# Kernel tuning notes

Measured on AMD Instinct MI355X. Metric: run time of the kernel, lower is better.

The kernel has to match this reference:

```python
import jax, jax.numpy as jnp
import numpy as np

D = 384      # d_model
H = 12       # num_heads
DK = 32      # head dim
L = 6        # num_layers
FF = 1536    # FFN intermediate (4*d_model)
EPS = 1e-12  # BERT LayerNorm eps


def layer_norm(x, w, b):
    m = jnp.mean(x, -1, keepdims=True)
    v = jnp.mean((x - m) ** 2, -1, keepdims=True)
    return (x - m) * jax.lax.rsqrt(v + EPS) * w + b


def deltanet(x, mask, Wq, bq, Wk, bk, Wv, bv, Wb, bb, Wg, bg, Wo, bo, fl, sl):
    # Hierarchical delta-rule linear attention with fast/slow decay states.
    B, S, _ = x.shape
    q = (x @ Wq + bq).reshape(B, S, H, DK)
    k = (x @ Wk + bk).reshape(B, S, H, DK)
    k = k / (jnp.linalg.norm(k, axis=-1, keepdims=True) + 1e-6)
    v = (x @ Wv + bv).reshape(B, S, H, DK)
    beta = jax.nn.sigmoid(x @ Wb + bb) * mask[:, :, None]   # [B,S,H] write gate
    g = jax.nn.sigmoid(x @ Wg + bg)                          # [B,S,H] flux mix gate
    af = jax.nn.sigmoid(fl)[None, :, None, None]             # fast decay, init 0.3
    as_ = jax.nn.sigmoid(sl)[None, :, None, None]            # slow decay, init 0.85

    def step(carry, inp):
        Sf, Ss = carry                      # [B,H,DK,DK] states
        qt, kt, vt, bt, gt = inp            # [B,H,DK],[B,H,DK],[B,H,DK],[B,H],[B,H]
        rf = jnp.einsum('bhkd,bhk->bhd', Sf, kt)
        Sf = af * Sf + bt[..., None, None] * kt[..., :, None] * (vt - rf)[:, :, None, :]
        of = jnp.einsum('bhkd,bhk->bhd', Sf, qt)
        rs = jnp.einsum('bhkd,bhk->bhd', Ss, kt)
        Ss = as_ * Ss + bt[..., None, None] * kt[..., :, None] * (vt - rs)[:, :, None, :]
        os_ = jnp.einsum('bhkd,bhk->bhd', Ss, qt)
        out = gt[..., None] * of + (1.0 - gt[..., None]) * os_
        return (Sf, Ss), out

    to_t = lambda a: jnp.moveaxis(a, 1, 0)  # [B,S,...] -> [S,B,...]
    S0 = jnp.zeros((B, H, DK, DK), x.dtype)
    _, out = jax.lax.scan(step, (S0, S0), (to_t(q), to_t(k), to_t(v), to_t(beta), to_t(g)))
    out = jnp.moveaxis(out, 0, 1).reshape(B, S, D)
    return out @ Wo + bo


def _forward(input_ids, attention_mask, word_emb, pos_emb, type_emb, emb_ln_w, emb_ln_b,
             Wq, bq, Wk, bk, Wv, bv, Wbeta, bbeta, Wg, bg, Wo, bo, fast_logit, slow_logit,
             attn_ln_w, attn_ln_b, ffn_w1, ffn_b1, ffn_w2, ffn_b2, ffn_ln_w, ffn_ln_b):
    B, S = input_ids.shape
    mask = attention_mask.astype(jnp.float32)
    x = word_emb[input_ids] + pos_emb[:S][None] + type_emb[0][None, None]
    x = layer_norm(x, emb_ln_w, emb_ln_b)
    for i in range(L):
        res = x
        a = deltanet(x, mask, Wq[i], bq[i], Wk[i], bk[i], Wv[i], bv[i],
                     Wbeta[i], bbeta[i], Wg[i], bg[i], Wo[i], bo[i],
                     fast_logit[i], slow_logit[i])
        x = layer_norm(res + a, attn_ln_w[i], attn_ln_b[i])
        res = x
        h = jax.nn.gelu(x @ ffn_w1[i] + ffn_b1[i], approximate=False)
        x = layer_norm(res + h @ ffn_w2[i] + ffn_b2[i], ffn_ln_w[i], ffn_ln_b[i])
    m = mask[:, :, None]
    emb = jnp.sum(x * m, 1) / jnp.clip(jnp.sum(m, 1), 1e-9)
    return emb / jnp.linalg.norm(emb, axis=1, keepdims=True)


def setup_inputs() -> dict:
    key = jax.random.key(0)
    ks = jax.random.split(key, 16)
    B, S, V, P = 64, 512, 30522, 512
    n = lambda k, shp, s=0.02: jax.random.normal(k, shp, jnp.float32) * s
    return {
        'input_ids': jax.random.randint(ks[0], (B, S), 0, V),
        'attention_mask': jnp.ones((B, S), jnp.int32),
        'word_emb': n(ks[1], (V, D)),
        'pos_emb': n(ks[2], (P, D)),
        'type_emb': n(ks[3], (2, D)),
        'emb_ln_w': jnp.ones((D,)), 'emb_ln_b': jnp.zeros((D,)),
        'Wq': n(ks[4], (L, D, D)), 'bq': jnp.zeros((L, D)),
        'Wk': n(ks[5], (L, D, D)), 'bk': jnp.zeros((L, D)),
        'Wv': n(ks[6], (L, D, D)), 'bv': jnp.zeros((L, D)),
        'Wbeta': n(ks[7], (L, D, H)), 'bbeta': jnp.zeros((L, H)),
        'Wg': n(ks[8], (L, D, H)), 'bg': jnp.zeros((L, H)),
        'Wo': n(ks[9], (L, D, D)), 'bo': jnp.zeros((L, D)),
        'fast_logit': jnp.full((L, H), -0.8473, jnp.float32),  # sigmoid -> 0.3
        'slow_logit': jnp.full((L, H), 1.7346, jnp.float32),   # sigmoid -> 0.85
        'attn_ln_w': jnp.ones((L, D)), 'attn_ln_b': jnp.zeros((L, D)),
        'ffn_w1': n(ks[10], (L, D, FF)), 'ffn_b1': jnp.zeros((L, FF)),
        'ffn_w2': n(ks[11], (L, FF, D)), 'ffn_b2': jnp.zeros((L, D)),
        'ffn_ln_w': jnp.ones((L, D)), 'ffn_ln_b': jnp.zeros((L, D)),
    }


def reference(input_ids, attention_mask, word_emb, pos_emb, type_emb, emb_ln_w, emb_ln_b,
              Wq, bq, Wk, bk, Wv, bv, Wbeta, bbeta, Wg, bg, Wo, bo, fast_logit, slow_logit,
              attn_ln_w, attn_ln_b, ffn_w1, ffn_b1, ffn_w2, ffn_b2, ffn_ln_w, ffn_ln_b):
    return _forward(input_ids, attention_mask, word_emb, pos_emb, type_emb, emb_ln_w, emb_ln_b,
                    Wq, bq, Wk, bk, Wv, bv, Wbeta, bbeta, Wg, bg, Wo, bo, fast_logit, slow_logit,
                    attn_ln_w, attn_ln_b, ffn_w1, ffn_b1, ffn_w2, ffn_b2, ffn_ln_w, ffn_ln_b)
```

## Files before the change

### kernel.cpp

```cpp
#include <hip/hip_runtime.h>
#include <math.h>

#define DD 384
#define HH 12
#define DKK 32
#define LL 6
#define FFF 1536
#define BB 64
#define SS 512
#define MROWS (BB*SS)
#define TB 32
#define LDX 1152

typedef _Float16 f16;
typedef _Float16 half8 __attribute__((ext_vector_type(8)));
typedef _Float16 h2 __attribute__((ext_vector_type(2)));
typedef float f32x4 __attribute__((ext_vector_type(4)));
typedef float f32x2 __attribute__((ext_vector_type(2)));

__device__ __forceinline__ float sigmoidf_(float x){ return 1.0f/(1.0f+expf(-x)); }

__device__ __forceinline__ float h2f_lo(unsigned int u){
  union { unsigned short s; f16 h; } c; c.s = (unsigned short)(u & 0xffffu); return (float)c.h;
}
__device__ __forceinline__ float h2f_hi(unsigned int u){
  union { unsigned short s; f16 h; } c; c.s = (unsigned short)(u >> 16); return (float)c.h;
}

__device__ __forceinline__ void gl2lds16(const void* g, void* l){
  __builtin_amdgcn_global_load_lds((const __attribute__((address_space(1))) void*)g,
                                   (__attribute__((address_space(3))) void*)l, 16, 0, 0);
}

__global__ __launch_bounds__(256) void embed_ln_kernel(
    const int* __restrict__ ids, const float* __restrict__ we,
    const float* __restrict__ pe, const float* __restrict__ te,
    const float* __restrict__ w, const float* __restrict__ b,
    float* __restrict__ x, f16* __restrict__ xh)
{
  int wv = threadIdx.x >> 6, lane = threadIdx.x & 63;
  int row = blockIdx.x * 4 + wv;
  int s = row & (SS-1);
  int id = ids[row];
  const float* wep = we + (size_t)id * DD;
  const float* pep = pe + (size_t)s * DD;
  float vals[6]; float sum = 0.f;
  #pragma unroll
  for (int i=0;i<6;i++){ int d = lane + 64*i; vals[i] = wep[d] + pep[d] + te[d]; sum += vals[i]; }
  #pragma unroll
  for (int off=32; off>=1; off>>=1) sum += __shfl_xor(sum, off);
  float mean = sum * (1.0f/DD);
  float vs = 0.f;
  #pragma unroll
  for (int i=0;i<6;i++){ float dv = vals[i]-mean; vs += dv*dv; }
  #pragma unroll
  for (int off=32; off>=1; off>>=1) vs += __shfl_xor(vs, off);
  float inv = rsqrtf(vs*(1.0f/DD) + 1e-12f);
  float* xr = x + (size_t)row*DD;
  f16* xhr = xh + (size_t)row*DD;
  #pragma unroll
  for (int i=0;i<6;i++){ int d = lane + 64*i; float o = (vals[i]-mean)*inv*w[d] + b[d]; xr[d]=o; xhr[d]=(f16)o; }
}

template<int YH>
__global__ __launch_bounds__(256) void add_ln_kernel(
    float* __restrict__ x, f16* __restrict__ xh, const void* __restrict__ yp,
    const float* __restrict__ w, const float* __restrict__ b, int row0, int ldy)
{
  int wv = threadIdx.x >> 6, lane = threadIdx.x & 63;
  int rrel = blockIdx.x * 4 + wv;
  int row = row0 + rrel;
  float* xr = x + (size_t)row*DD;
  f16* xhr = xh + (size_t)row*DD;
  float vals[6]; float sum = 0.f;
  #pragma unroll
  for (int i=0;i<6;i++){
    int d = lane + 64*i;
    float yv;
    if (YH) yv = (float)((const f16*)yp)[(size_t)rrel*ldy + d];
    else    yv = ((const float*)yp)[(size_t)rrel*ldy + d];
    vals[i] = xr[d] + yv; sum += vals[i];
  }
  #pragma unroll
  for (int off=32; off>=1; off>>=1) sum += __shfl_xor(sum, off);
  float mean = sum * (1.0f/DD);
  float vs = 0.f;
  #pragma unroll
  for (int i=0;i<6;i++){ float dv = vals[i]-mean; vs += dv*dv; }
  #pragma unroll
  for (int off=32; off>=1; off>>=1) vs += __shfl_xor(vs, off);
  float inv = rsqrtf(vs*(1.0f/DD) + 1e-12f);
  #pragma unroll
  for (int i=0;i<6;i++){ int d = lane + 64*i; float o = (vals[i]-mean)*inv*w[d] + b[d]; xr[d]=o; xhr[d]=(f16)o; }
}

__global__ __launch_bounds__(256) void biaspack_kernel(
    const float* __restrict__ bq, const float* __restrict__ bk, const float* __restrict__ bv,
    float* __restrict__ dst)
{
  int i = blockIdx.x*256 + threadIdx.x;
  if (i >= LL*LDX) return;
  int l = i / LDX, r = i - l*LDX;
  float v;
  if (r < 384) v = bq[l*DD + r];
  else if (r < 768) v = bk[l*DD + r-384];
  else v = bv[l*DD + r-768];
  dst[i] = v;
}

__global__ __launch_bounds__(256) void wtrans_kernel(
  const float* __restrict__ Wq, const float* __restrict__ Wk, const float* __restrict__ Wv,
  const float* __restrict__ Wo, const float* __restrict__ W1, const float* __restrict__ W2,
  f16* __restrict__ Wt)
{
  __shared__ float T[32][33];
  int l = blockIdx.x / 1728, bidx = blockIdx.x % 1728;
  const float* src; f16* dst; int K, N, tile;
  if (bidx < 576){ int m = bidx/144; tile = bidx - m*144; K=384; N=384;
    const float* w4[4] = {Wq + (size_t)l*147456, Wk + (size_t)l*147456,
                          Wv + (size_t)l*147456, Wo + (size_t)l*147456};
    src = w4[m]; dst = Wt + (size_t)l*1769472 + m*147456; }
  else if (bidx < 1152){ tile = bidx-576; K=384; N=1536;
    src = W1 + (size_t)l*589824; dst = Wt + (size_t)l*1769472 + 589824; }
  else { tile = bidx-1152; K=1536; N=384;
    src = W2 + (size_t)l*589824; dst = Wt + (size_t)l*1769472 + 1179648; }
  int tN = N>>5;
  int tk = tile / tN, tn = tile - tk*tN;
  int k0 = tk<<5, n0 = tn<<5;
  int r = threadIdx.x >> 3, c4 = (threadIdx.x & 7) << 2;
  float4 vv = *(const float4*)(src + (size_t)(k0+r)*N + n0 + c4);
  T[r][c4+0]=vv.x; T[r][c4+1]=vv.y; T[r][c4+2]=vv.z; T[r][c4+3]=vv.w;
  __syncthreads();
  f16* dp = dst + (size_t)(n0+r)*K + k0 + c4;
  #pragma unroll
  for (int j=0;j<4;j++) dp[j] = (f16)T[c4+j][r];
}

template<int ACT, int OUT16>
__global__ __launch_bounds__(256) void gemm_f16(
    const f16* __restrict__ A, const f16* __restrict__ BT,
    const float* __restrict__ bias, float* __restrict__ Cf, f16* __restrict__ Ch,
    int M, int N, int K, int lda, int ldc)
{
  __shared__ __align__(16) f16 As0[128*32];
  __shared__ __align__(16) f16 As1[128*32];
  __shared__ __align__(16) f16 Bs0[128*32];
  __shared__ __align__(16) f16 Bs1[128*32];
  int tid = threadIdx.x, lane = tid & 63, wave = tid >> 6;
  int wm = wave >> 1, wn = wave & 1;
  int n0 = blockIdx.x * 128, m0 = blockIdx.y * 128;
  f32x4 acc[4][4] = {};
  int seg0 = wave*2048 + lane*16;
  int ar = lane & 15, kq = (lane >> 4) * 8;

  for (int k0=0; k0<K; k0+=64){
    #pragma unroll
    for (int i=0;i<2;i++){
      int seg = seg0 + i*1024;
      int e = seg >> 1; int row = e >> 5; int kk = e & 31;
      const f16* ap = A  + (size_t)(m0+row)*lda + k0 + kk;
      const f16* bp = BT + (size_t)(n0+row)*K   + k0 + kk;
      gl2lds16(ap,      (char*)As0 + seg);
      gl2lds16(ap + 32, (char*)As1 + seg);
      gl2lds16(bp,      (char*)Bs0 + seg);
      gl2lds16(bp + 32, (char*)Bs1 + seg);
    }
    __syncthreads();
    {
      half8 af[4], bf[4];
      #pragma unroll
      for (int mi=0;mi<4;mi++) af[mi] = *(const half8*)&As0[(wm*64 + mi*16 + ar)*32 + kq];
      #pragma unroll
      for (int ni=0;ni<4;ni++) bf[ni] = *(const half8*)&Bs0[(wn*64 + ni*16 + ar)*32 + kq];
      #pragma unroll
      for (int mi=0;mi<4;mi++)
        #pragma unroll
        for (int ni=0;ni<4;ni++)
          acc[mi][ni] = __builtin_amdgcn_mfma_f32_16x16x32_f16(af[mi], bf[ni], acc[mi][ni], 0, 0, 0);
    }
    {
      half8 af[4], bf[4];
      #pragma unroll
      for (int mi=0;mi<4;mi++) af[mi] = *(const half8*)&As1[(wm*64 + mi*16 + ar)*32 + kq];
      #pragma unroll
      for (int ni=0;ni<4;ni++) bf[ni] = *(const half8*)&Bs1[(wn*64 + ni*16 + ar)*32 + kq];
      #pragma unroll
      for (int mi=0;mi<4;mi++)
        #pragma unroll
        for (int ni=0;ni<4;ni++)
          acc[mi][ni] = __builtin_amdgcn_mfma_f32_16x16x32_f16(af[mi], bf[ni], acc[mi][ni], 0, 0, 0);
    }
    __syncthreads();
  }
  int rb = (lane >> 4) * 4, cb = lane & 15;
  #pragma unroll
  for (int ni=0;ni<4;ni++){
    int cn = n0 + wn*64 + ni*16 + cb;
    float bz = bias[cn];
    #pragma unroll
    for (int mi=0;mi<4;mi++){
      int rm = m0 + wm*64 + mi*16 + rb;
      #pragma unroll
      for (int r=0;r<4;r++){
        float v = acc[mi][ni][r] + bz;
        if (ACT==1) v = 0.5f*v*(1.0f+erff(v*0.70710678118f));
        if (OUT16) Ch[(size_t)(rm+r)*ldc + cn] = (f16)v;
        else       Cf[(size_t)(rm+r)*ldc + cn] = v;
      }
    }
  }
}

__global__ __launch_bounds__(256) void betag_kernel(
    const float* __restrict__ x, const float* __restrict__ Wb, const float* __restrict__ bb,
    const float* __restrict__ Wg, const float* __restrict__ bg,
    const int* __restrict__ mask, float* __restrict__ beta, float* __restrict__ g)
{
  __shared__ float Ws[384*25];
  for (int idx = threadIdx.x; idx < 384*12; idx += 256){
    int k = idx/12, j = idx - k*12;
    Ws[k*25+j]    = Wb[idx];
    Ws[k*25+12+j] = Wg[idx];
  }
  __syncthreads();
  int wv = threadIdx.x>>6, lane = threadIdx.x&63;
  int row = blockIdx.x*4 + wv;
  const float* xr = x + (size_t)row*DD;
  float accb[12], accg[12];
  #pragma unroll
  for (int j=0;j<12;j++){ accb[j]=0.f; accg[j]=0.f; }
  #pragma unroll
  for (int i=0;i<6;i++){
    int k = lane + 64*i;
    float xv = xr[k];
    const float* wr = &Ws[k*25];
    #pragma unroll
    for (int j=0;j<12;j++){ accb[j] += xv*wr[j]; accg[j] += xv*wr[12+j]; }
  }
  #pragma unroll
  for (int j=0;j<12;j++){
    #pragma unroll
    for (int off=32; off>=1; off>>=1){
      accb[j]+=__shfl_xor(accb[j],off);
      accg[j]+=__shfl_xor(accg[j],off);
    }
  }
  if (lane==0){
    float mk = (float)mask[row];
    #pragma unroll
    for (int j=0;j<12;j++){
      beta[(size_t)row*HH + j] = sigmoidf_(accb[j]+bb[j]) * mk;
      g[(size_t)row*HH + j]    = sigmoidf_(accg[j]+bg[j]);
    }
  }
}

__global__ __launch_bounds__(64) void scan_kernel(
  f16* qkv,
  const float* __restrict__ bp, const float* __restrict__ gp,
  const float* __restrict__ flp, const float* __restrict__ slp)
{
  __shared__ float Kf[2][TB][32];
  __shared__ float Qf[2][TB][32];
  __shared__ float Vf[2][TB][32];
  __shared__ float Bg[2][2][TB];
  __shared__ float Of[TB][64];
  int blk = blockIdx.x;
  int b = blk / HH, h = blk - b*HH;
  int lane = threadIdx.x;
  int col = lane & 31;
  float a = sigmoidf_((lane < 32) ? flp[h] : slp[h]);
  f32x2 a2 = {a, a};
  f32x2 S2[16];
  #pragma unroll
  for (int j=0;j<16;j++) S2[j] = (f32x2){0.f,0.f};
  size_t base = ((size_t)b*SS)*LDX + (size_t)h*DKK;
  f16* qb = qkv + base;
  const f16* kb = qkv + base + 384;
  const f16* vb = qkv + base + 768;
  const float* bbp = bp + ((size_t)b*SS)*HH + h;
  const float* gbp = gp + ((size_t)b*SS)*HH + h;

  int st0 = lane >> 2, part = lane & 3;
  uint4 kv[2], qv[2], vv[2]; float bgv;

  #define LOADG(T0) do {                                                       \
    _Pragma("unroll")                                                          \
    for (int r=0;r<2;r++){                                                     \
      int st = (T0) + r*16 + st0;                                              \
      size_t off = (size_t)st*LDX + part*8;                                    \
      kv[r] = *(const uint4*)(kb + off);                                       \
      qv[r] = *(const uint4*)(qb + off);                                       \
      vv[r] = *(const uint4*)(vb + off);                                       \
    }                                                                          \
    int tb_ = (T0) + (lane & 31);                                              \
    bgv = (lane < 32) ? bbp[(size_t)tb_*HH] : gbp[(size_t)tb_*HH];             \
  } while(0)

  #define STAGE(BUF) do {                                                      \
    _Pragma("unroll")                                                          \
    for (int r=0;r<2;r++){                                                     \
      int s = r*16 + st0;                                                      \
      float kf[8], qf[8], vf[8];                                               \
      kf[0]=h2f_lo(kv[r].x); kf[1]=h2f_hi(kv[r].x); kf[2]=h2f_lo(kv[r].y);     \
      kf[3]=h2f_hi(kv[r].y); kf[4]=h2f_lo(kv[r].z); kf[5]=h2f_hi(kv[r].z);     \
      kf[6]=h2f_lo(kv[r].w); kf[7]=h2f_hi(kv[r].w);                            \
      qf[0]=h2f_lo(qv[r].x); qf[1]=h2f_hi(qv[r].x); qf[2]=h2f_lo(qv[r].y);     \
      qf[3]=h2f_hi(qv[r].y); qf[4]=h2f_lo(qv[r].z); qf[5]=h2f_hi(qv[r].z);     \
      qf[6]=h2f_lo(qv[r].w); qf[7]=h2f_hi(qv[r].w);                            \
      vf[0]=h2f_lo(vv[r].x); vf[1]=h2f_hi(vv[r].x); vf[2]=h2f_lo(vv[r].y);     \
      vf[3]=h2f_hi(vv[r].y); vf[4]=h2f_lo(vv[r].z); vf[5]=h2f_hi(vv[r].z);     \
      vf[6]=h2f_lo(vv[r].w); vf[7]=h2f_hi(vv[r].w);                            \
      float ss = 0.f;                                                          \
      _Pragma("unroll")                                                        \
      for (int i=0;i<8;i++) ss += kf[i]*kf[i];                                 \
      ss += __shfl_xor(ss, 1); ss += __shfl_xor(ss, 2);                        \
      float sc = 1.0f/(sqrtf(ss)+1e-6f);                                       \
      float4 t;                                                                \
      t.x=kf[0]*sc; t.y=kf[1]*sc; t.z=kf[2]*sc; t.w=kf[3]*sc;                  \
      *(float4*)&Kf[BUF][s][part*8] = t;                                       \
      t.x=kf[4]*sc; t.y=kf[5]*sc; t.z=kf[6]*sc; t.w=kf[7]*sc;                  \
      *(float4*)&Kf[BUF][s][part*8+4] = t;                                     \
      t.x=qf[0]; t.y=qf[1]; t.z=qf[2]; t.w=qf[3];                              \
      *(float4*)&Qf[BUF][s][part*8] = t;                                       \
      t.x=qf[4]; t.y=qf[5]; t.z=qf[6]; t.w=qf[7];                              \
      *(float4*)&Qf[BUF][s][part*8+4] = t;                                     \
      t.x=vf[0]; t.y=vf[1]; t.z=vf[2]; t.w=vf[3];                              \
      *(float4*)&Vf[BUF][s][part*8] = t;                                       \
      t.x=vf[4]; t.y=vf[5]; t.z=vf[6]; t.w=vf[7];                              \
      *(float4*)&Vf[BUF][s][part*8+4] = t;                                     \
    }                                                                          \
    Bg[BUF][lane>>5][lane&31] = bgv;                                           \
  } while(0)

  #define LDSTEP(BUF,S,KR,QR,VT,BT) do {                                       \
    const float4* k4_ = (const float4*)&Kf[BUF][S][0];                         \
    const float4* q4_ = (const float4*)&Qf[BUF][S][0];                         \
    _Pragma("unroll")                                                          \
    for (int j=0;j<8;j++){ KR[j]=k4_[j]; QR[j]=q4_[j]; }                       \
    VT = Vf[BUF][S][col]; BT = Bg[BUF][0][S];                                  \
  } while(0)

  #define STEP(KR,QR,VT,BT,S) do {                                            \
    const f32x2* k2_ = (const f32x2*)KR;                                       \
    const f32x2* q2_ = (const f32x2*)QR;                                       \
    f32x2 rA={0.f,0.f},rB={0.f,0.f},rC={0.f,0.f},rD={0.f,0.f};                 \
    _Pragma("unroll")                                                          \
    for (int j=0;j<16;j+=4){                                                   \
      rA += S2[j+0]*k2_[j+0]; rB += S2[j+1]*k2_[j+1];                          \
      rC += S2[j+2]*k2_[j+2]; rD += S2[j+3]*k2_[j+3]; }                        \
    f32x2 rr = (rA+rB)+(rC+rD);                                                \
    float rf = rr.x + rr.y;                                                    \
    float c_ = (BT)*((VT) - rf);                                               \
    f32x2 c2 = {c_, c_};                                                       \
    _Pragma("unroll")                                                          \
    for (int j=0;j<16;j++) S2[j] = a2*S2[j] + c2*k2_[j];                       \
    f32x2 oA={0.f,0.f},oB={0.f,0.f},oC={0.f,0.f},oD={0.f,0.f};                 \
    _Pragma("unroll")                                                          \
    for (int j=0;j<16;j+=4){                                                   \
      oA += S2[j+0]*q2_[j+0]; oB += S2[j+1]*q2_[j+1];                          \
      oC += S2[j+2]*q2_[j+2]; oD += S2[j+3]*q2_[j+3]; }                        \
    f32x2 oo = (oA+oB)+(oC+oD);                                                \
    Of[S][lane] = oo.x + oo.y;                                                 \
  } while(0)

  #define COMBINE(BUF,T0) do {                                                 \
    _Pragma("unroll")                                                          \
    for (int i=0;i<16;i++){                                                    \
      int idx = i*64 + lane;                                                   \
      int s_ = idx >> 5, c_ = idx & 31;                                        \
      float fv = Of[s_][c_];                                                   \
      float sv = Of[s_][c_+32];                                                \
      float gv = Bg[BUF][1][s_];                                               \
      qb[(size_t)((T0)+s_)*LDX + c_] = (f16)(gv*fv + (1.0f-gv)*sv);            \
    }                                                                          \
  } while(0)

  LOADG(0);
  STAGE(0);
  __syncthreads();

  float4 kA[8], qA[8], kB[8], qB[8];
  float vA, bA, vB, bB;

  for (int tile=0; tile<SS/TB; tile++){
    int buf = tile & 1;
    if (tile < SS/TB-1) LOADG((tile+1)*TB);
    LDSTEP(buf, 0, kA, qA, vA, bA);
    #pragma unroll
    for (int s=0; s<TB; s+=2){
      if (s+1 < TB) LDSTEP(buf, s+1, kB, qB, vB, bB);
      STEP(kA, qA, vA, bA, s);
      if (s+2 < TB) LDSTEP(buf, s+2, kA, qA, vA, bA);
      STEP(kB, qB, vB, bB, s+1);
    }
    if (tile < SS/TB-1) STAGE(1-buf);
    COMBINE(buf, tile*TB);
    __syncthreads();
  }
  #undef LOADG
  #undef STAGE
  #undef LDSTEP
  #undef STEP
  #undef COMBINE
}

__global__ __launch_bounds__(384) void pool_kernel(
    const float* __restrict__ x, const int* __restrict__ mask, float* __restrict__ out)
{
  __shared__ float red[384];
  __shared__ float tot;
  int b = blockIdx.x, d = threadIdx.x;
  const float* xb = x + (size_t)b*SS*DD;
  const int* mb = mask + b*SS;
  float s=0.f, sm=0.f;
  for (int t=0;t<SS;t++){ float m=(float)mb[t]; s += xb[(size_t)t*DD+d]*m; sm += m; }
  float emb = s / fmaxf(sm, 1e-9f);
  red[d] = emb*emb;
  __syncthreads();
  for (int off=192; off>=3; off>>=1){
    if (d < off) red[d] += red[d+off];
    __syncthreads();
  }
  if (d==0) tot = red[0]+red[1]+red[2];
  __syncthreads();
  out[(size_t)b*DD + d] = emb * rsqrtf(tot);
}

extern "C" void kernel_launch(void* const* d_in, const int* in_sizes, int n_in,
                              void* d_out, int out_size, void* d_ws, size_t ws_size,
                              hipStream_t stream)
{
  const int*   ids  = (const int*)d_in[0];
  const int*   amask= (const int*)d_in[1];
  const float* we   = (const float*)d_in[2];
  const float* pe   = (const float*)d_in[3];
  const float* te   = (const float*)d_in[4];
  const float* elnw = (const float*)d_in[5];
  const float* elnb = (const float*)d_in[6];
  const float* Wq   = (const float*)d_in[7];
  const float* bq   = (const float*)d_in[8];
  const float* Wk   = (const float*)d_in[9];
  const float* bk   = (const float*)d_in[10];
  const float* Wv   = (const float*)d_in[11];
  const float* bv   = (const float*)d_in[12];
  const float* Wb   = (const float*)d_in[13];
  const float* bb   = (const float*)d_in[14];
  const float* Wg   = (const float*)d_in[15];
  const float* bgp  = (const float*)d_in[16];
  const float* Wo   = (const float*)d_in[17];
  const float* bo   = (const float*)d_in[18];
  const float* fl   = (const float*)d_in[19];
  const float* sl   = (const float*)d_in[20];
  const float* alnw = (const float*)d_in[21];
  const float* alnb = (const float*)d_in[22];
  const float* W1   = (const float*)d_in[23];
  const float* b1   = (const float*)d_in[24];
  const float* W2   = (const float*)d_in[25];
  const float* b2   = (const float*)d_in[26];
  const float* flnw = (const float*)d_in[27];
  const float* flnb = (const float*)d_in[28];
  float* out = (float*)d_out;
  float* w = (float*)d_ws;

  float* x    = w;
  f16*  xh   = (f16*)(w + 12582912);
  f16*  qkvh = (f16*)(w + 18874368);
  float* f2   = w + 37748736;
  f16*  f2h  = (f16*)f2;
  float* beta = f2 + 3145728;
  float* gbuf = beta + 393216;
  f16*  wt   = (f16*)(w + 44040192);
  float* bqkv = w + 49348608;
  f16*  hbf  = qkvh;

  embed_ln_kernel<<<MROWS/4, 256, 0, stream>>>(ids, we, pe, te, elnw, elnb, x, xh);
  biaspack_kernel<<<27,256,0,stream>>>(bq, bk, bv, bqkv);
  wtrans_kernel<<<LL*1728,256,0,stream>>>(Wq, Wk, Wv, Wo, W1, W2, wt);

  for (int l=0;l<LL;l++){
    f16* wl = wt + (size_t)l*1769472;

    gemm_f16<0,1><<<dim3(9,256),256,0,stream>>>(xh, wl, bqkv + l*LDX, nullptr, qkvh,
                                                MROWS, LDX, DD, DD, LDX);

    betag_kernel<<<MROWS/4,256,0,stream>>>(x, Wb + (size_t)l*DD*HH, bb + l*HH,
                                           Wg + (size_t)l*DD*HH, bgp + l*HH,
                                           amask, beta, gbuf);
    scan_kernel<<<BB*HH,64,0,stream>>>(qkvh, beta, gbuf, fl + l*HH, sl + l*HH);

    gemm_f16<0,1><<<dim3(3,256),256,0,stream>>>(qkvh, wl+442368, bo+l*DD, nullptr,
                                                qkvh + 384, MROWS, DD, DD, LDX, LDX);
    add_ln_kernel<1><<<MROWS/4,256,0,stream>>>(x, xh, qkvh + 384, alnw+l*DD, alnb+l*DD, 0, LDX);

    for (int c=0;c<2;c++){
      gemm_f16<1,1><<<dim3(12,128),256,0,stream>>>(xh + (size_t)c*16384*DD, wl+589824,
                                                   b1+l*FFF, nullptr, hbf, 16384, FFF, DD, DD, FFF);
      gemm_f16<0,1><<<dim3(3,128),256,0,stream>>>(hbf, wl+1179648, b2+l*DD, nullptr, f2h,
                                                  16384, DD, FFF, FFF, DD);
      add_ln_kernel<1><<<4096,256,0,stream>>>(x, xh, f2h, flnw+l*DD, flnb+l*DD, c*16384, DD);
    }
  }

  pool_kernel<<<BB,384,0,stream>>>(x, amask, out);
}
```

Baseline: 3.604 ms.

## Split scan state across four waves with shuffle-reduced k and q dot products

The delta-rule scan kernel goes from one 64-thread wave per (batch, head) to 256 threads. Each wave holds one state (fast or slow) and half of the value columns, and each lane keeps 8 state elements instead of 32. The dot products are finished with two xor-shuffles per step. Staging and combine are spread across all 256 threads, and an extra barrier is added before restaging. The aim is to shorten the serial per-timestep critical path and raise occupancy (768 blocks of 64 threads could not fill the GPU well). In exchange it adds shuffle latency on every step and an extra block-wide synchronisation per tile.

```diff
diff --git a/kernel.cpp b/kernel.cpp
--- a/kernel.cpp
+++ b/kernel.cpp
@@ -255,7 +255,7 @@
   }
 }
 
-__global__ __launch_bounds__(64) void scan_kernel(
+__global__ __launch_bounds__(256) void scan_kernel(
   f16* qkv,
   const float* __restrict__ bp, const float* __restrict__ gp,
   const float* __restrict__ flp, const float* __restrict__ slp)
@@ -267,13 +267,21 @@
   __shared__ float Of[TB][64];
   int blk = blockIdx.x;
   int b = blk / HH, h = blk - b*HH;
-  int lane = threadIdx.x;
-  int col = lane & 31;
-  float a = sigmoidf_((lane < 32) ? flp[h] : slp[h]);
+  int tid  = threadIdx.x;
+  int lane = tid & 63;
+  int wave = tid >> 6;
+  int state = wave >> 1;
+  int colh  = wave & 1;
+  int kq2   = (lane & 3) * 2;
+  int dcol  = colh*16 + (lane >> 2);
+  int ofs   = state*32 + dcol;
+
+  float a = sigmoidf_((state == 0) ? flp[h] : slp[h]);
   f32x2 a2 = {a, a};
-  f32x2 S2[16];
-  #pragma unroll
-  for (int j=0;j<16;j++) S2[j] = (f32x2){0.f,0.f};
+  f32x2 S2[4];
+  #pragma unroll
+  for (int j=0;j<4;j++) S2[j] = (f32x2){0.f,0.f};
+
   size_t base = ((size_t)b*SS)*LDX + (size_t)h*DKK;
   f16* qb = qkv + base;
   const f16* kb = qkv + base + 384;
@@ -281,93 +289,67 @@
   const float* bbp = bp + ((size_t)b*SS)*HH + h;
   const float* gbp = gp + ((size_t)b*SS)*HH + h;
 
-  int st0 = lane >> 2, part = lane & 3;
-  uint4 kv[2], qv[2], vv[2]; float bgv;
+  uint2 kv, qv, vv; float bgv = 0.f;
 
   #define LOADG(T0) do {                                                       \
-    _Pragma("unroll")                                                          \
-    for (int r=0;r<2;r++){                                                     \
-      int st = (T0) + r*16 + st0;                                              \
-      size_t off = (size_t)st*LDX + part*8;                                    \
-      kv[r] = *(const uint4*)(kb + off);                                       \
-      qv[r] = *(const uint4*)(qb + off);                                       \
-      vv[r] = *(const uint4*)(vb + off);                                       \
-    }                                                                          \
-    int tb_ = (T0) + (lane & 31);                                              \
-    bgv = (lane < 32) ? bbp[(size_t)tb_*HH] : gbp[(size_t)tb_*HH];             \
+    int s_ = tid >> 3, part_ = tid & 7;                                        \
+    size_t off = (size_t)((T0)+s_)*LDX + part_*4;                              \
+    kv = *(const uint2*)(kb + off);                                            \
+    qv = *(const uint2*)(qb + off);                                            \
+    vv = *(const uint2*)(vb + off);                                            \
+    if (tid < 64)                                                              \
+      bgv = (tid < 32) ? bbp[(size_t)((T0)+tid)*HH]                            \
+                       : gbp[(size_t)((T0)+tid-32)*HH];                        \
   } while(0)
 
   #define STAGE(BUF) do {                                                      \
-    _Pragma("unroll")                                                          \
-    for (int r=0;r<2;r++){                                                     \
-      int s = r*16 + st0;                                                      \
-      float kf[8], qf[8], vf[8];                                               \
-      kf[0]=h2f_lo(kv[r].x); kf[1]=h2f_hi(kv[r].x); kf[2]=h2f_lo(kv[r].y);     \
-      kf[3]=h2f_hi(kv[r].y); kf[4]=h2f_lo(kv[r].z); kf[5]=h2f_hi(kv[r].z);     \
-      kf[6]=h2f_lo(kv[r].w); kf[7]=h2f_hi(kv[r].w);                            \
-      qf[0]=h2f_lo(qv[r].x); qf[1]=h2f_hi(qv[r].x); qf[2]=h2f_lo(qv[r].y);     \
-      qf[3]=h2f_hi(qv[r].y); qf[4]=h2f_lo(qv[r].z); qf[5]=h2f_hi(qv[r].z);     \
-      qf[6]=h2f_lo(qv[r].w); qf[7]=h2f_hi(qv[r].w);                            \
-      vf[0]=h2f_lo(vv[r].x); vf[1]=h2f_hi(vv[r].x); vf[2]=h2f_lo(vv[r].y);     \
-      vf[3]=h2f_hi(vv[r].y); vf[4]=h2f_lo(vv[r].z); vf[5]=h2f_hi(vv[r].z);     \
-      vf[6]=h2f_lo(vv[r].w); vf[7]=h2f_hi(vv[r].w);                            \
-      float ss = 0.f;                                                          \
-      _Pragma("unroll")                                                        \
-      for (int i=0;i<8;i++) ss += kf[i]*kf[i];                                 \
-      ss += __shfl_xor(ss, 1); ss += __shfl_xor(ss, 2);                        \
-      float sc = 1.0f/(sqrtf(ss)+1e-6f);                                       \
-      float4 t;                                                                \
-      t.x=kf[0]*sc; t.y=kf[1]*sc; t.z=kf[2]*sc; t.w=kf[3]*sc;                  \
-      *(float4*)&Kf[BUF][s][part*8] = t;                                       \
-      t.x=kf[4]*sc; t.y=kf[5]*sc; t.z=kf[6]*sc; t.w=kf[7]*sc;                  \
-      *(float4*)&Kf[BUF][s][part*8+4] = t;                                     \
-      t.x=qf[0]; t.y=qf[1]; t.z=qf[2]; t.w=qf[3];                              \
-      *(float4*)&Qf[BUF][s][part*8] = t;                                       \
-      t.x=qf[4]; t.y=qf[5]; t.z=qf[6]; t.w=qf[7];                              \
-      *(float4*)&Qf[BUF][s][part*8+4] = t;                                     \
-      t.x=vf[0]; t.y=vf[1]; t.z=vf[2]; t.w=vf[3];                              \
-      *(float4*)&Vf[BUF][s][part*8] = t;                                       \
-      t.x=vf[4]; t.y=vf[5]; t.z=vf[6]; t.w=vf[7];                              \
-      *(float4*)&Vf[BUF][s][part*8+4] = t;                                     \
-    }                                                                          \
-    Bg[BUF][lane>>5][lane&31] = bgv;                                           \
+    int s_ = tid >> 3, part_ = tid & 7;                                        \
+    float kf0=h2f_lo(kv.x), kf1=h2f_hi(kv.x), kf2=h2f_lo(kv.y), kf3=h2f_hi(kv.y); \
+    float ss = kf0*kf0 + kf1*kf1 + kf2*kf2 + kf3*kf3;                          \
+    ss += __shfl_xor(ss, 1); ss += __shfl_xor(ss, 2); ss += __shfl_xor(ss, 4); \
+    float sc = 1.0f/(sqrtf(ss)+1e-6f);                                         \
+    float4 t;                                                                  \
+    t.x=kf0*sc; t.y=kf1*sc; t.z=kf2*sc; t.w=kf3*sc;                            \
+    *(float4*)&Kf[BUF][s_][part_*4] = t;                                       \
+    t.x=h2f_lo(qv.x); t.y=h2f_hi(qv.x); t.z=h2f_lo(qv.y); t.w=h2f_hi(qv.y);    \
+    *(float4*)&Qf[BUF][s_][part_*4] = t;                                       \
+    t.x=h2f_lo(vv.x); t.y=h2f_hi(vv.x); t.z=h2f_lo(vv.y); t.w=h2f_hi(vv.y);    \
+    *(float4*)&Vf[BUF][s_][part_*4] = t;                                       \
+    if (tid < 64) Bg[BUF][tid>>5][tid&31] = bgv;                               \
   } while(0)
 
   #define LDSTEP(BUF,S,KR,QR,VT,BT) do {                                       \
     const float4* k4_ = (const float4*)&Kf[BUF][S][0];                         \
     const float4* q4_ = (const float4*)&Qf[BUF][S][0];                         \
-    _Pragma("unroll")                                                          \
-    for (int j=0;j<8;j++){ KR[j]=k4_[j]; QR[j]=q4_[j]; }                       \
-    VT = Vf[BUF][S][col]; BT = Bg[BUF][0][S];                                  \
+    KR[0]=k4_[kq2]; KR[1]=k4_[kq2+1];                                          \
+    QR[0]=q4_[kq2]; QR[1]=q4_[kq2+1];                                          \
+    VT = Vf[BUF][S][dcol]; BT = Bg[BUF][0][S];                                 \
   } while(0)
 
   #define STEP(KR,QR,VT,BT,S) do {                                            \
     const f32x2* k2_ = (const f32x2*)KR;                                       \
     const f32x2* q2_ = (const f32x2*)QR;                                       \
-    f32x2 rA={0.f,0.f},rB={0.f,0.f},rC={0.f,0.f},rD={0.f,0.f};                 \
-    _Pragma("unroll")                                                          \
-    for (int j=0;j<16;j+=4){                                                   \
-      rA += S2[j+0]*k2_[j+0]; rB += S2[j+1]*k2_[j+1];                          \
-      rC += S2[j+2]*k2_[j+2]; rD += S2[j+3]*k2_[j+3]; }                        \
-    f32x2 rr = (rA+rB)+(rC+rD);                                                \
+    f32x2 rA = S2[0]*k2_[0]; f32x2 rB = S2[1]*k2_[1];                          \
+    rA += S2[2]*k2_[2];      rB += S2[3]*k2_[3];                               \
+    f32x2 rr = rA + rB;                                                        \
     float rf = rr.x + rr.y;                                                    \
+    rf += __shfl_xor(rf, 1); rf += __shfl_xor(rf, 2);                          \
     float c_ = (BT)*((VT) - rf);                                               \
     f32x2 c2 = {c_, c_};                                                       \
-    _Pragma("unroll")                                                          \
-    for (int j=0;j<16;j++) S2[j] = a2*S2[j] + c2*k2_[j];                       \
-    f32x2 oA={0.f,0.f},oB={0.f,0.f},oC={0.f,0.f},oD={0.f,0.f};                 \
-    _Pragma("unroll")                                                          \
-    for (int j=0;j<16;j+=4){                                                   \
-      oA += S2[j+0]*q2_[j+0]; oB += S2[j+1]*q2_[j+1];                          \
-      oC += S2[j+2]*q2_[j+2]; oD += S2[j+3]*q2_[j+3]; }                        \
-    f32x2 oo = (oA+oB)+(oC+oD);                                                \
-    Of[S][lane] = oo.x + oo.y;                                                 \
+    S2[0] = a2*S2[0] + c2*k2_[0]; S2[1] = a2*S2[1] + c2*k2_[1];                \
+    S2[2] = a2*S2[2] + c2*k2_[2]; S2[3] = a2*S2[3] + c2*k2_[3];                \
+    f32x2 oA = S2[0]*q2_[0]; f32x2 oB = S2[1]*q2_[1];                          \
+    oA += S2[2]*q2_[2];      oB += S2[3]*q2_[3];                               \
+    f32x2 oo = oA + oB;                                                        \
+    float o_ = oo.x + oo.y;                                                    \
+    o_ += __shfl_xor(o_, 1); o_ += __shfl_xor(o_, 2);                          \
+    if ((lane & 3) == 0) Of[S][ofs] = o_;                                      \
   } while(0)
 
   #define COMBINE(BUF,T0) do {                                                 \
     _Pragma("unroll")                                                          \
-    for (int i=0;i<16;i++){                                                    \
-      int idx = i*64 + lane;                                                   \
+    for (int i=0;i<4;i++){                                                     \
+      int idx = i*256 + tid;                                                   \
       int s_ = idx >> 5, c_ = idx & 31;                                        \
       float fv = Of[s_][c_];                                                   \
       float sv = Of[s_][c_+32];                                                \
@@ -380,7 +362,7 @@
   STAGE(0);
   __syncthreads();
 
-  float4 kA[8], qA[8], kB[8], qB[8];
+  float4 kA[2], qA[2], kB[2], qB[2];
   float vA, bA, vB, bB;
 
   for (int tile=0; tile<SS/TB; tile++){
@@ -394,6 +376,7 @@
       if (s+2 < TB) LDSTEP(buf, s+2, kA, qA, vA, bA);
       STEP(kB, qB, vB, bB, s+1);
     }
+    __syncthreads();
     if (tile < SS/TB-1) STAGE(1-buf);
     COMBINE(buf, tile*TB);
     __syncthreads();
@@ -487,7 +470,7 @@
     betag_kernel<<<MROWS/4,256,0,stream>>>(x, Wb + (size_t)l*DD*HH, bb + l*HH,
                                            Wg + (size_t)l*DD*HH, bgp + l*HH,
                                            amask, beta, gbuf);
-    scan_kernel<<<BB*HH,64,0,stream>>>(qkvh, beta, gbuf, fl + l*HH, sl + l*HH);
+    scan_kernel<<<BB*HH,256,0,stream>>>(qkvh, beta, gbuf, fl + l*HH, sl + l*HH);
 
     gemm_f16<0,1><<<dim3(3,256),256,0,stream>>>(qkvh, wl+442368, bo+l*DD, nullptr,
                                                 qkvh + 384, MROWS, DD, DD, LDX, LDX);
```

Result: faster. 3.492 ms (-3.1%).

## Split key dimension across wave halves in delta-rule scan kernel

Applied to the files above, without the earlier changes.

The scan kernel used to give lanes 0-31 the full fast-decay state and lanes 32-63 the full slow-decay state. Now each half of the wave holds half of the key dimension for both the fast and the slow state. Partial dot products are combined with cross-half shuffles (`__shfl_xor(..., 32)`). This halves the per-step LDS reads of k and q and shortens each serial dot-product chain. The cost is cross-lane shuffle latency on the recurrence's critical path: three shuffles per timestep, one of them needed before the state update can start.

```diff
diff --git a/kernel.cpp b/kernel.cpp
--- a/kernel.cpp
+++ b/kernel.cpp
@@ -268,12 +268,18 @@
   int blk = blockIdx.x;
   int b = blk / HH, h = blk - b*HH;
   int lane = threadIdx.x;
-  int col = lane & 31;
-  float a = sigmoidf_((lane < 32) ? flp[h] : slp[h]);
-  f32x2 a2 = {a, a};
-  f32x2 S2[16];
-  #pragma unroll
-  for (int j=0;j<16;j++) S2[j] = (f32x2){0.f,0.f};
+  int col  = lane & 31;
+  int khalf = lane >> 5;
+  int kq0 = khalf*4;
+  int ofs = khalf*32 + col;
+
+  float afv = sigmoidf_(flp[h]);
+  float asv = sigmoidf_(slp[h]);
+  f32x2 af2 = {afv, afv}, as2 = {asv, asv};
+  f32x2 Sf[8], Ss[8];
+  #pragma unroll
+  for (int j=0;j<8;j++){ Sf[j] = (f32x2){0.f,0.f}; Ss[j] = (f32x2){0.f,0.f}; }
+
   size_t base = ((size_t)b*SS)*LDX + (size_t)h*DKK;
   f16* qb = qkv + base;
   const f16* kb = qkv + base + 384;
@@ -336,32 +342,50 @@
   #define LDSTEP(BUF,S,KR,QR,VT,BT) do {                                       \
     const float4* k4_ = (const float4*)&Kf[BUF][S][0];                         \
     const float4* q4_ = (const float4*)&Qf[BUF][S][0];                         \
-    _Pragma("unroll")                                                          \
-    for (int j=0;j<8;j++){ KR[j]=k4_[j]; QR[j]=q4_[j]; }                       \
+    KR[0]=k4_[kq0]; KR[1]=k4_[kq0+1]; KR[2]=k4_[kq0+2]; KR[3]=k4_[kq0+3];      \
+    QR[0]=q4_[kq0]; QR[1]=q4_[kq0+1]; QR[2]=q4_[kq0+2]; QR[3]=q4_[kq0+3];      \
     VT = Vf[BUF][S][col]; BT = Bg[BUF][0][S];                                  \
   } while(0)
 
   #define STEP(KR,QR,VT,BT,S) do {                                            \
     const f32x2* k2_ = (const f32x2*)KR;                                       \
     const f32x2* q2_ = (const f32x2*)QR;                                       \
-    f32x2 rA={0.f,0.f},rB={0.f,0.f},rC={0.f,0.f},rD={0.f,0.f};                 \
+    f32x2 fA = Sf[0]*k2_[0]; f32x2 fB = Sf[1]*k2_[1];                          \
+    f32x2 sA = Ss[0]*k2_[0]; f32x2 sB = Ss[1]*k2_[1];                          \
+    fA += Sf[2]*k2_[2]; fB += Sf[3]*k2_[3];                                    \
+    sA += Ss[2]*k2_[2]; sB += Ss[3]*k2_[3];                                    \
+    fA += Sf[4]*k2_[4]; fB += Sf[5]*k2_[5];                                    \
+    sA += Ss[4]*k2_[4]; sB += Ss[5]*k2_[5];                                    \
+    fA += Sf[6]*k2_[6]; fB += Sf[7]*k2_[7];                                    \
+    sA += Ss[6]*k2_[6]; sB += Ss[7]*k2_[7];                                    \
+    f32x2 fT = fA + fB; f32x2 sT = sA + sB;                                    \
+    float pf = fT.x + fT.y;                                                    \
+    float ps = sT.x + sT.y;                                                    \
+    float rf = pf + __shfl_xor(pf, 32);                                        \
+    float rs = ps + __shfl_xor(ps, 32);                                        \
+    float cf_ = (BT)*((VT) - rf);                                              \
+    float cs_ = (BT)*((VT) - rs);                                              \
+    f32x2 cf2 = {cf_, cf_}, cs2 = {cs_, cs_};                                  \
     _Pragma("unroll")                                                          \
-    for (int j=0;j<16;j+=4){                                                   \
-      rA += S2[j+0]*k2_[j+0]; rB += S2[j+1]*k2_[j+1];                          \
-      rC += S2[j+2]*k2_[j+2]; rD += S2[j+3]*k2_[j+3]; }                        \
-    f32x2 rr = (rA+rB)+(rC+rD);                                                \
-    float rf = rr.x + rr.y;                                                    \
-    float c_ = (BT)*((VT) - rf);                                               \
-    f32x2 c2 = {c_, c_};                                                       \
-    _Pragma("unroll")                                                          \
-    for (int j=0;j<16;j++) S2[j] = a2*S2[j] + c2*k2_[j];                       \
-    f32x2 oA={0.f,0.f},oB={0.f,0.f},oC={0.f,0.f},oD={0.f,0.f};                 \
-    _Pragma("unroll")                                                          \
-    for (int j=0;j<16;j+=4){                                                   \
-      oA += S2[j+0]*q2_[j+0]; oB += S2[j+1]*q2_[j+1];                          \
-      oC += S2[j+2]*q2_[j+2]; oD += S2[j+3]*q2_[j+3]; }                        \
-    f32x2 oo = (oA+oB)+(oC+oD);                                                \
-    Of[S][lane] = oo.x + oo.y;                                                 \
+    for (int j=0;j<8;j++){                                                     \
+      Sf[j] = af2*Sf[j] + cf2*k2_[j];                                          \
+      Ss[j] = as2*Ss[j] + cs2*k2_[j];                                          \
+    }                                                                          \
+    f32x2 oA = Sf[0]*q2_[0]; f32x2 oB = Sf[1]*q2_[1];                          \
+    f32x2 uA = Ss[0]*q2_[0]; f32x2 uB = Ss[1]*q2_[1];                          \
+    oA += Sf[2]*q2_[2]; oB += Sf[3]*q2_[3];                                    \
+    uA += Ss[2]*q2_[2]; uB += Ss[3]*q2_[3];                                    \
+    oA += Sf[4]*q2_[4]; oB += Sf[5]*q2_[5];                                    \
+    uA += Ss[4]*q2_[4]; uB += Ss[5]*q2_[5];                                    \
+    oA += Sf[6]*q2_[6]; oB += Sf[7]*q2_[7];                                    \
+    uA += Ss[6]*q2_[6]; uB += Ss[7]*q2_[7];                                    \
+    f32x2 oT = oA + oB; f32x2 uT = uA + uB;                                    \
+    float of_p = oT.x + oT.y;                                                  \
+    float os_p = uT.x + uT.y;                                                  \
+    float send_ = khalf ? of_p : os_p;                                         \
+    float recv_ = __shfl_xor(send_, 32);                                       \
+    float o_ = (khalf ? os_p : of_p) + recv_;                                  \
+    Of[S][ofs] = o_;                                                           \
   } while(0)
 
   #define COMBINE(BUF,T0) do {                                                 \
@@ -380,7 +404,7 @@
   STAGE(0);
   __syncthreads();
 
-  float4 kA[8], qA[8], kB[8], qB[8];
+  float4 kA[4], qA[4], kB[4], qB[4];
   float vA, bA, vB, bB;
 
   for (int tile=0; tile<SS/TB; tile++){
```

Result: no change. 3.596 ms (-0.2%).
